# Kernel tuning notes

Hardware: AMD Instinct MI355X
Metric: run time of the kernel (lower is better)

Reference implementation:

```python
import jax, jax.numpy as jnp
import numpy as np

B, S, D, H = 2, 2048, 1024, 16
HD = D // H

def setup_inputs() -> dict:
    key = jax.random.key(0)
    ks = jax.random.split(key, 5)
    scale = 0.02
    return {
        "x": jax.random.normal(ks[0], (B, S, D), dtype=jnp.float32),
        "Wq": jax.random.normal(ks[1], (D, D), dtype=jnp.float32) * scale,
        "Wk": jax.random.normal(ks[2], (D, D), dtype=jnp.float32) * scale,
        "Wv": jax.random.normal(ks[3], (D, D), dtype=jnp.float32) * scale,
        "Wo": jax.random.normal(ks[4], (D, D), dtype=jnp.float32) * scale,
        "bo": jnp.zeros((D,), dtype=jnp.float32),
    }

def reference(x, Wq, Wk, Wv, Wo, bo):
    b, n, _ = x.shape
    h, hd = H, HD
    # QKV projections (torch Linear: x @ W.T)
    q = (x @ Wq.T).reshape(b, n, h, hd).transpose(0, 2, 1, 3)  # [b,h,n,hd]
    k = (x @ Wk.T).reshape(b, n, h, hd).transpose(0, 2, 1, 3)
    v = (x @ Wv.T).reshape(b, n, h, hd).transpose(0, 2, 1, 3)
    scores = jnp.einsum("bhqd,bhkd->bhqk", q, k) / jnp.sqrt(jnp.float32(hd))
    # causal mask: positions j > i masked out
    causal = jnp.tril(jnp.ones((n, n), dtype=bool))
    scores = jnp.where(causal, scores, jnp.float32(-jnp.inf))
    attn = jax.nn.softmax(scores, axis=-1)  # dropout p=0.0 (eval)
    ctx = jnp.einsum("bhqk,bhkd->bhqd", attn, v)
    ctx = ctx.transpose(0, 2, 1, 3).reshape(b, n, h * hd)
    return ctx @ Wo.T + bo
```

## Files before the change

kernel.cpp:

```cpp
#include <hip/hip_runtime.h>
#include <stdint.h>

typedef __attribute__((ext_vector_type(8))) short short8;
typedef __attribute__((ext_vector_type(4))) short s16x4;
typedef __attribute__((ext_vector_type(4))) float f32x4;
typedef __attribute__((ext_vector_type(4))) uint32_t u32x4;

#define B_ 2
#define S_ 2048
#define D_ 1024
#define H_ 16
#define HD_ 64
#define BS_ (B_ * S_)
#define QKVN (3 * D_)
#define QKN 2048
#define XN8 (BS_ * D_ / 8)
#define WN8 (D_ * D_ / 8)

#define NEGBIG (-1e30f)

__device__ __forceinline__ short f2bf(float f) {
    uint32_t u = __builtin_bit_cast(uint32_t, f);
    u = (u + 0x7FFFu + ((u >> 16) & 1u)) >> 16;
    return (short)u;
}

__device__ __forceinline__ uint32_t cvtpk_bf16(float lo, float hi) {
    uint32_t r;
    asm("v_cvt_pk_bf16_f32 %0, %1, %2" : "=v"(r) : "v"(lo), "v"(hi));
    return r;
}

__device__ __forceinline__ void gload_lds16(const void* g, void* lds) {
    __builtin_amdgcn_global_load_lds(
        (const __attribute__((address_space(1))) void*)g,
        (__attribute__((address_space(3))) void*)lds, 16, 0, 0);
}

__global__ void castall(const float* __restrict__ x, const float* __restrict__ Wq,
                        const float* __restrict__ Wk, const float* __restrict__ Wv,
                        const float* __restrict__ Wo, short* __restrict__ dst,
                        float qs) {
    int i = blockIdx.x * blockDim.x + threadIdx.x;
    int stride = gridDim.x * blockDim.x;
    const int total = XN8 + 4 * WN8;
    for (; i < total; i += stride) {
        const float* s;
        int loc;
        float sc = 1.f;
        if (i < XN8) {
            s = x; loc = i;
        } else {
            int r = i - XN8;
            int wi = r >> 17;
            loc = r & (WN8 - 1);
            s = (wi == 0) ? Wq : (wi == 1) ? Wk : (wi == 2) ? Wv : Wo;
            if (wi == 0) sc = qs;
        }
        const float* sp = s + (size_t)loc * 8;
        short8 o;
#pragma unroll
        for (int j = 0; j < 8; ++j) o[j] = f2bf(sp[j] * sc);
        *(short8*)(dst + (size_t)i * 8) = o;
    }
}

template <int MODE>
__global__ __launch_bounds__(256) void gemm_nt(
    const short* __restrict__ A, const short* __restrict__ Bt,
    void* __restrict__ Cout, const float* __restrict__ bias,
    short* __restrict__ vtg, int M, int N, int K) {
    __shared__ short As[128 * 64];
    __shared__ short Bs[128 * 64];
    const int tid = threadIdx.x;
    const int w = tid >> 6, l = tid & 63;
    const int lg = l >> 4, lr = l & 15;
    const int nbn = N >> 7;
    const int bm = blockIdx.x / nbn, bn = blockIdx.x % nbn;
    const int m0 = bm << 7, n0 = bn << 7;
    const int wm = (w >> 1) << 6, wn = (w & 1) << 6;

    f32x4 acc[4][4] = {};

    for (int kt = 0; kt < K; kt += 64) {
#pragma unroll
        for (int it = 0; it < 4; ++it) {
            int off = ((it * 4 + w) * 64 + l) * 16;
            int row = off >> 7;
            int scol = (off & 127) ^ ((row & 7) << 4);
            gload_lds16(A + (size_t)(m0 + row) * K + kt + (scol >> 1),
                        (char*)As + (it * 4 + w) * 1024);
            gload_lds16(Bt + (size_t)(n0 + row) * K + kt + (scol >> 1),
                        (char*)Bs + (it * 4 + w) * 1024);
        }
        __syncthreads();
        short8 af[4][2], bf[4][2];
#pragma unroll
        for (int f = 0; f < 4; ++f)
#pragma unroll
            for (int ks = 0; ks < 2; ++ks) {
                int ra = wm + f * 16 + lr;
                af[f][ks] = *(const short8*)((const char*)As + ra * 128 +
                                             ((lg * 16 + ks * 64) ^ ((ra & 7) << 4)));
                int rb = wn + f * 16 + lr;
                bf[f][ks] = *(const short8*)((const char*)Bs + rb * 128 +
                                             ((lg * 16 + ks * 64) ^ ((rb & 7) << 4)));
            }
#pragma unroll
        for (int mf = 0; mf < 4; ++mf)
#pragma unroll
            for (int nf = 0; nf < 4; ++nf)
#pragma unroll
                for (int ks = 0; ks < 2; ++ks)
                    acc[mf][nf] = __builtin_amdgcn_mfma_f32_16x16x32_bf16(
                        af[mf][ks], bf[nf][ks], acc[mf][nf], 0, 0, 0);
        __syncthreads();
    }

    if (MODE == 2 && n0 >= QKN) {
#pragma unroll
        for (int mf = 0; mf < 4; ++mf)
#pragma unroll
            for (int nf = 0; nf < 4; ++nf) {
                int col = n0 + wn + nf * 16 + lr - QKN;
                int hh = col >> 6, d = col & 63;
                int token = m0 + wm + mf * 16 + lg * 4;
                int b = token >> 11, tk = token & 2047;
                int t64 = tk & ~63, rem = tk & 63;
                int r32 = rem & 31;
                int pos = (rem >> 5) * 32 + ((r32 & 15) >> 2) * 8 + ((r32 >> 4) & 1) * 4;
                s16x4 o;
#pragma unroll
                for (int i = 0; i < 4; ++i) o[i] = f2bf(acc[mf][nf][i]);
                *(s16x4*)&vtg[((size_t)(b * 16 + hh) * 64 + d) * (size_t)S_ + t64 + pos] = o;
            }
        return;
    }

#pragma unroll
    for (int mf = 0; mf < 4; ++mf)
#pragma unroll
        for (int nf = 0; nf < 4; ++nf) {
            int col = n0 + wn + nf * 16 + lr;
            float bv = 0.f;
            if (MODE == 1) bv = bias[col];
#pragma unroll
            for (int i = 0; i < 4; ++i) {
                int row = m0 + wm + mf * 16 + lg * 4 + i;
                float v = acc[mf][nf][i] + bv;
                if (MODE == 1)
                    ((float*)Cout)[(size_t)row * N + col] = v;
                else
                    ((short*)Cout)[(size_t)row * QKN + col] = f2bf(v);
            }
        }
}

__global__ __launch_bounds__(256) void attn_fwd(const short* __restrict__ qkb,
                                                const short* __restrict__ vtg,
                                                short* __restrict__ ctx) {
    const int qt = (S_ / 64 - 1) - blockIdx.x;
    const int bh = blockIdx.y;
    const int b = bh >> 4, h = bh & 15;
    const int tid = threadIdx.x;
    const int w = tid >> 6, l = tid & 63;
    const int lg = l >> 4, lr = l & 15;
    const int q0w = qt * 64 + w * 16;

    __shared__ short Ks[2][64 * 64];
    __shared__ short Vt[2][64 * 64];

    const short* base = qkb + (size_t)(b * S_) * QKN + h * HD_;
    const short* kpg = base + D_;
    const short* vrow = vtg + (size_t)bh * 64 * S_;

    short8 qf[2];
    {
        const short* g = base + (size_t)(q0w + lr) * QKN + lg * 8;
        qf[0] = *(const short8*)g;
        qf[1] = *(const short8*)(g + 32);
    }

    int off0 = (w * 64 + l) * 16, off1 = ((4 + w) * 64 + l) * 16;
    int row0 = off0 >> 7, row1 = off1 >> 7;
    int sc0 = (off0 & 127) ^ ((row0 & 7) << 4);
    int sc1 = (off1 & 127) ^ ((row1 & 7) << 4);
    const short* kA = kpg + (size_t)row0 * QKN + (sc0 >> 1);
    const short* kB = kpg + (size_t)row1 * QKN + (sc1 >> 1);
    const short* vA = vrow + (size_t)row0 * S_ + (sc0 >> 1);
    const short* vB = vrow + (size_t)row1 * S_ + (sc1 >> 1);
    char* ldsKA[2] = {(char*)Ks[0] + w * 1024, (char*)Ks[1] + w * 1024};
    char* ldsKB[2] = {(char*)Ks[0] + (4 + w) * 1024, (char*)Ks[1] + (4 + w) * 1024};
    char* ldsVA[2] = {(char*)Vt[0] + w * 1024, (char*)Vt[1] + w * 1024};
    char* ldsVB[2] = {(char*)Vt[0] + (4 + w) * 1024, (char*)Vt[1] + (4 + w) * 1024};

    auto stage = [&](int buf) {
        gload_lds16(kA, ldsKA[buf]);
        gload_lds16(kB, ldsKB[buf]);
        gload_lds16(vA, ldsVA[buf]);
        gload_lds16(vB, ldsVB[buf]);
        kA += 64 * QKN; kB += 64 * QKN; vA += 64; vB += 64;
    };

    float m2 = NEGBIG, lsum = 0.f;
    f32x4 cacc[4] = {};
    const int qabs = q0w + lr;

    stage(0);
    __syncthreads();

    for (int kt = 0; kt <= qt; ++kt) {
        const int buf = kt & 1;
        if (kt < qt) stage(buf ^ 1);

        const char* ksb = (const char*)Ks[buf];
        const char* vtb = (const char*)Vt[buf];

        f32x4 sfr[4] = {};
#pragma unroll
        for (int f = 0; f < 4; ++f)
#pragma unroll
            for (int ks = 0; ks < 2; ++ks) {
                int r = f * 16 + lr;
                short8 kf = *(const short8*)(ksb + r * 128 +
                                             ((lg * 16 + ks * 64) ^ ((r & 7) << 4)));
                sfr[f] = __builtin_amdgcn_mfma_f32_16x16x32_bf16(kf, qf[ks], sfr[f], 0, 0, 0);
            }

        float p[16];
        if (kt == qt) {
            const int kb = kt * 64;
#pragma unroll
            for (int f = 0; f < 4; ++f)
#pragma unroll
                for (int i = 0; i < 4; ++i) {
                    int kpo = kb + f * 16 + lg * 4 + i;
                    p[f * 4 + i] = (kpo <= qabs) ? sfr[f][i] : NEGBIG;
                }
        } else {
#pragma unroll
            for (int f = 0; f < 4; ++f)
#pragma unroll
                for (int i = 0; i < 4; ++i) p[f * 4 + i] = sfr[f][i];
        }
        float mx01 = fmaxf(fmaxf(p[0], p[1]), fmaxf(p[2], p[3]));
        float mx23 = fmaxf(fmaxf(p[4], p[5]), fmaxf(p[6], p[7]));
        float mx45 = fmaxf(fmaxf(p[8], p[9]), fmaxf(p[10], p[11]));
        float mx67 = fmaxf(fmaxf(p[12], p[13]), fmaxf(p[14], p[15]));
        float tmax = fmaxf(fmaxf(mx01, mx23), fmaxf(mx45, mx67));

        if (!__all(tmax - m2 <= 8.f)) {
            float rmax = fmaxf(tmax, __shfl_xor(tmax, 16));
            rmax = fmaxf(rmax, __shfl_xor(rmax, 32));
            float mnew = fmaxf(m2, rmax);
            float crs = exp2f(m2 - mnew);
            m2 = mnew;
            lsum *= crs;
#pragma unroll
            for (int i = 0; i < 4; ++i) {
                float ci = __shfl(crs, lg * 4 + i);
#pragma unroll
                for (int nf = 0; nf < 4; ++nf) cacc[nf][i] *= ci;
            }
        }
#pragma unroll
        for (int t = 0; t < 16; ++t) p[t] = exp2f(p[t] - m2);
        float s0 = (p[0] + p[1]) + (p[2] + p[3]);
        float s1 = (p[4] + p[5]) + (p[6] + p[7]);
        float s2 = (p[8] + p[9]) + (p[10] + p[11]);
        float s3 = (p[12] + p[13]) + (p[14] + p[15]);
        lsum += (s0 + s1) + (s2 + s3);

        short8 pa[2];
#pragma unroll
        for (int ks = 0; ks < 2; ++ks) {
            u32x4 pw;
#pragma unroll
            for (int wd = 0; wd < 4; ++wd) {
                int tb = (2 * ks + (wd >> 1)) * 4 + (wd & 1) * 2;
                pw[wd] = cvtpk_bf16(p[tb], p[tb + 1]);
            }
            pa[ks] = __builtin_bit_cast(short8, pw);
        }

#pragma unroll
        for (int nf = 0; nf < 4; ++nf) {
            int r = nf * 16 + lr;
#pragma unroll
            for (int ks = 0; ks < 2; ++ks) {
                short8 vf = *(const short8*)(vtb + r * 128 +
                                             ((ks * 64 + lg * 16) ^ ((r & 7) << 4)));
                cacc[nf] = __builtin_amdgcn_mfma_f32_16x16x32_bf16(pa[ks], vf, cacc[nf], 0, 0, 0);
            }
        }
        __syncthreads();
    }

    lsum += __shfl_xor(lsum, 16);
    lsum += __shfl_xor(lsum, 32);
    float inv = 1.0f / lsum;
#pragma unroll
    for (int i = 0; i < 4; ++i) {
        float li = __shfl(inv, lg * 4 + i);
        int srow = q0w + lg * 4 + i;
        short* o = ctx + (size_t)(b * S_ + srow) * D_ + h * HD_ + lr;
#pragma unroll
        for (int nf = 0; nf < 4; ++nf) o[nf * 16] = f2bf(cacc[nf][i] * li);
    }
}

extern "C" void kernel_launch(void* const* d_in, const int* in_sizes, int n_in,
                              void* d_out, int out_size, void* d_ws, size_t ws_size,
                              hipStream_t stream) {
    const float* x  = (const float*)d_in[0];
    const float* Wq = (const float*)d_in[1];
    const float* Wk = (const float*)d_in[2];
    const float* Wv = (const float*)d_in[3];
    const float* Wo = (const float*)d_in[4];
    const float* bo = (const float*)d_in[5];

    short* xb   = (short*)d_ws;
    short* Wqkv = xb + (size_t)BS_ * D_;
    short* Wob  = Wqkv + (size_t)QKVN * D_;
    short* qkb  = Wob + (size_t)D_ * D_;
    short* ctxb = qkb + (size_t)BS_ * QKN;
    short* vtg  = ctxb + (size_t)BS_ * D_;

    const float qscale = 0.125f * 1.44269504089f;
    castall<<<2048, 256, 0, stream>>>(x, Wq, Wk, Wv, Wo, (short*)d_ws, qscale);

    gemm_nt<2><<<dim3((BS_ / 128) * (QKVN / 128)), 256, 0, stream>>>(
        xb, Wqkv, qkb, nullptr, vtg, BS_, QKVN, D_);

    attn_fwd<<<dim3(S_ / 64, B_ * H_), 256, 0, stream>>>(qkb, vtg, ctxb);

    gemm_nt<1><<<dim3((BS_ / 128) * (D_ / 128)), 256, 0, stream>>>(
        ctxb, Wob, d_out, bo, nullptr, BS_, D_, D_);
}
```

Measured before the change: 217.2 us.

## Pair high and low causal query tiles per attention block to share K/V loads

Each attention block now handles two query tiles, one near the end of the sequence and its mirror near the start, giving every block the same amount of causal work. Each staged K/V tile is reused for both query tiles while the low tile is still active, which halves the K/V traffic for that stretch and halves the grid size. The K and V fragments are preloaded into registers, and exp2f is replaced with the raw v_exp_f32 instruction. The cost is higher register pressure from two sets of accumulators, and a grid of only 512 blocks may leave some compute units underused.

New measurement: 187.7 us. -13.6%, faster.

```diff
diff --git a/kernel.cpp b/kernel.cpp
--- a/kernel.cpp
+++ b/kernel.cpp
@@ -28,6 +28,12 @@
 __device__ __forceinline__ uint32_t cvtpk_bf16(float lo, float hi) {
     uint32_t r;
     asm("v_cvt_pk_bf16_f32 %0, %1, %2" : "=v"(r) : "v"(lo), "v"(hi));
+    return r;
+}
+
+__device__ __forceinline__ float vexp2(float x) {
+    float r;
+    asm("v_exp_f32 %0, %1" : "=v"(r) : "v"(x));
     return r;
 }
 
@@ -159,26 +165,29 @@
 __global__ __launch_bounds__(256) void attn_fwd(const short* __restrict__ qkb,
                                                 const short* __restrict__ vtg,
                                                 short* __restrict__ ctx) {
-    const int qt = (S_ / 64 - 1) - blockIdx.x;
+    const int bx = blockIdx.x;
+    const int qtH = (S_ / 64 - 1) - bx;
+    const int qtL = bx;
     const int bh = blockIdx.y;
     const int b = bh >> 4, h = bh & 15;
     const int tid = threadIdx.x;
     const int w = tid >> 6, l = tid & 63;
     const int lg = l >> 4, lr = l & 15;
-    const int q0w = qt * 64 + w * 16;
-
-    __shared__ short Ks[2][64 * 64];
-    __shared__ short Vt[2][64 * 64];
+
+    __shared__ __align__(16) char lds[32768];
 
     const short* base = qkb + (size_t)(b * S_) * QKN + h * HD_;
     const short* kpg = base + D_;
     const short* vrow = vtg + (size_t)bh * 64 * S_;
 
-    short8 qf[2];
+    short8 qfH[2], qfL[2];
     {
-        const short* g = base + (size_t)(q0w + lr) * QKN + lg * 8;
-        qf[0] = *(const short8*)g;
-        qf[1] = *(const short8*)(g + 32);
+        const short* g = base + (size_t)(qtH * 64 + w * 16 + lr) * QKN + lg * 8;
+        qfH[0] = *(const short8*)g;
+        qfH[1] = *(const short8*)(g + 32);
+        const short* g2 = base + (size_t)(qtL * 64 + w * 16 + lr) * QKN + lg * 8;
+        qfL[0] = *(const short8*)g2;
+        qfL[1] = *(const short8*)(g2 + 32);
     }
 
     int off0 = (w * 64 + l) * 16, off1 = ((4 + w) * 64 + l) * 16;
@@ -189,124 +198,145 @@
     const short* kB = kpg + (size_t)row1 * QKN + (sc1 >> 1);
     const short* vA = vrow + (size_t)row0 * S_ + (sc0 >> 1);
     const short* vB = vrow + (size_t)row1 * S_ + (sc1 >> 1);
-    char* ldsKA[2] = {(char*)Ks[0] + w * 1024, (char*)Ks[1] + w * 1024};
-    char* ldsKB[2] = {(char*)Ks[0] + (4 + w) * 1024, (char*)Ks[1] + (4 + w) * 1024};
-    char* ldsVA[2] = {(char*)Vt[0] + w * 1024, (char*)Vt[1] + w * 1024};
-    char* ldsVB[2] = {(char*)Vt[0] + (4 + w) * 1024, (char*)Vt[1] + (4 + w) * 1024};
+    const int dK0 = w * 1024, dK1 = (4 + w) * 1024;
 
     auto stage = [&](int buf) {
-        gload_lds16(kA, ldsKA[buf]);
-        gload_lds16(kB, ldsKB[buf]);
-        gload_lds16(vA, ldsVA[buf]);
-        gload_lds16(vB, ldsVB[buf]);
+        char* p = lds + (buf << 14);
+        gload_lds16(kA, p + dK0);
+        gload_lds16(kB, p + dK1);
+        gload_lds16(vA, p + 8192 + dK0);
+        gload_lds16(vB, p + 8192 + dK1);
         kA += 64 * QKN; kB += 64 * QKN; vA += 64; vB += 64;
     };
 
-    float m2 = NEGBIG, lsum = 0.f;
-    f32x4 cacc[4] = {};
-    const int qabs = q0w + lr;
+    const int xorp = (lr & 7) << 4;
+    const int ka0 = lr * 128 + ((lg * 16) ^ xorp);
+    const int ka1 = lr * 128 + ((lg * 16 + 64) ^ xorp);
+    const int va0 = 8192 + ka0;
+    const int va1 = 8192 + ka1;
+
+    float mH = NEGBIG, lsH = 0.f, mL = NEGBIG, lsL = 0.f;
+    f32x4 caccH[4] = {}, caccL[4] = {};
+    const int qrow = w * 16 + lr;
+    const int qabsH = qtH * 64 + qrow;
+    const int qabsL = qtL * 64 + qrow;
 
     stage(0);
     __syncthreads();
 
-    for (int kt = 0; kt <= qt; ++kt) {
+    for (int kt = 0; kt <= qtH; ++kt) {
         const int buf = kt & 1;
-        if (kt < qt) stage(buf ^ 1);
-
-        const char* ksb = (const char*)Ks[buf];
-        const char* vtb = (const char*)Vt[buf];
-
-        f32x4 sfr[4] = {};
-#pragma unroll
-        for (int f = 0; f < 4; ++f)
+        if (kt < qtH) stage(buf ^ 1);
+        const char* bb = lds + (buf << 14);
+        const bool doL = (kt <= qtL);
+
+        short8 kf[4][2];
+#pragma unroll
+        for (int f = 0; f < 4; ++f) {
+            kf[f][0] = *(const short8*)(bb + ka0 + f * 2048);
+            kf[f][1] = *(const short8*)(bb + ka1 + f * 2048);
+        }
+        f32x4 sH[4] = {};
+#pragma unroll
+        for (int f = 0; f < 4; ++f) {
+            sH[f] = __builtin_amdgcn_mfma_f32_16x16x32_bf16(kf[f][0], qfH[0], sH[f], 0, 0, 0);
+            sH[f] = __builtin_amdgcn_mfma_f32_16x16x32_bf16(kf[f][1], qfH[1], sH[f], 0, 0, 0);
+        }
+        f32x4 sL[4] = {};
+        if (doL) {
+#pragma unroll
+            for (int f = 0; f < 4; ++f) {
+                sL[f] = __builtin_amdgcn_mfma_f32_16x16x32_bf16(kf[f][0], qfL[0], sL[f], 0, 0, 0);
+                sL[f] = __builtin_amdgcn_mfma_f32_16x16x32_bf16(kf[f][1], qfL[1], sL[f], 0, 0, 0);
+            }
+        }
+        short8 vf[4][2];
+#pragma unroll
+        for (int nf = 0; nf < 4; ++nf) {
+            vf[nf][0] = *(const short8*)(bb + va0 + nf * 2048);
+            vf[nf][1] = *(const short8*)(bb + va1 + nf * 2048);
+        }
+
+        auto smpv = [&](f32x4(&sfr)[4], float& m2, float& lsum, f32x4(&cacc)[4],
+                        int qabs, bool diag) {
+            float p[16];
+            if (diag) {
+                int rel = qabs - kt * 64;
+#pragma unroll
+                for (int f = 0; f < 4; ++f)
+#pragma unroll
+                    for (int i = 0; i < 4; ++i)
+                        p[f * 4 + i] = (f * 16 + lg * 4 + i <= rel) ? sfr[f][i] : NEGBIG;
+            } else {
+#pragma unroll
+                for (int f = 0; f < 4; ++f)
+#pragma unroll
+                    for (int i = 0; i < 4; ++i) p[f * 4 + i] = sfr[f][i];
+            }
+            float t0 = fmaxf(fmaxf(p[0], p[1]), fmaxf(p[2], p[3]));
+            float t1 = fmaxf(fmaxf(p[4], p[5]), fmaxf(p[6], p[7]));
+            float t2 = fmaxf(fmaxf(p[8], p[9]), fmaxf(p[10], p[11]));
+            float t3 = fmaxf(fmaxf(p[12], p[13]), fmaxf(p[14], p[15]));
+            float tmax = fmaxf(fmaxf(t0, t1), fmaxf(t2, t3));
+            if (!__all(tmax - m2 <= 8.f)) {
+                float rmax = fmaxf(tmax, __shfl_xor(tmax, 16));
+                rmax = fmaxf(rmax, __shfl_xor(rmax, 32));
+                float mnew = fmaxf(m2, rmax);
+                float crs = vexp2(m2 - mnew);
+                m2 = mnew;
+                lsum *= crs;
+#pragma unroll
+                for (int i = 0; i < 4; ++i) {
+                    float ci = __shfl(crs, lg * 4 + i);
+#pragma unroll
+                    for (int nf = 0; nf < 4; ++nf) cacc[nf][i] *= ci;
+                }
+            }
+#pragma unroll
+            for (int t = 0; t < 16; ++t) p[t] = vexp2(p[t] - m2);
+            float s0 = (p[0] + p[1]) + (p[2] + p[3]);
+            float s1 = (p[4] + p[5]) + (p[6] + p[7]);
+            float s2 = (p[8] + p[9]) + (p[10] + p[11]);
+            float s3 = (p[12] + p[13]) + (p[14] + p[15]);
+            lsum += (s0 + s1) + (s2 + s3);
+            short8 pa[2];
 #pragma unroll
             for (int ks = 0; ks < 2; ++ks) {
-                int r = f * 16 + lr;
-                short8 kf = *(const short8*)(ksb + r * 128 +
-                                             ((lg * 16 + ks * 64) ^ ((r & 7) << 4)));
-                sfr[f] = __builtin_amdgcn_mfma_f32_16x16x32_bf16(kf, qf[ks], sfr[f], 0, 0, 0);
-            }
-
-        float p[16];
-        if (kt == qt) {
-            const int kb = kt * 64;
-#pragma unroll
-            for (int f = 0; f < 4; ++f)
-#pragma unroll
-                for (int i = 0; i < 4; ++i) {
-                    int kpo = kb + f * 16 + lg * 4 + i;
-                    p[f * 4 + i] = (kpo <= qabs) ? sfr[f][i] : NEGBIG;
+                u32x4 pw;
+#pragma unroll
+                for (int wd = 0; wd < 4; ++wd) {
+                    int tb = (2 * ks + (wd >> 1)) * 4 + (wd & 1) * 2;
+                    pw[wd] = cvtpk_bf16(p[tb], p[tb + 1]);
                 }
-        } else {
-#pragma unroll
-            for (int f = 0; f < 4; ++f)
-#pragma unroll
-                for (int i = 0; i < 4; ++i) p[f * 4 + i] = sfr[f][i];
-        }
-        float mx01 = fmaxf(fmaxf(p[0], p[1]), fmaxf(p[2], p[3]));
-        float mx23 = fmaxf(fmaxf(p[4], p[5]), fmaxf(p[6], p[7]));
-        float mx45 = fmaxf(fmaxf(p[8], p[9]), fmaxf(p[10], p[11]));
-        float mx67 = fmaxf(fmaxf(p[12], p[13]), fmaxf(p[14], p[15]));
-        float tmax = fmaxf(fmaxf(mx01, mx23), fmaxf(mx45, mx67));
-
-        if (!__all(tmax - m2 <= 8.f)) {
-            float rmax = fmaxf(tmax, __shfl_xor(tmax, 16));
-            rmax = fmaxf(rmax, __shfl_xor(rmax, 32));
-            float mnew = fmaxf(m2, rmax);
-            float crs = exp2f(m2 - mnew);
-            m2 = mnew;
-            lsum *= crs;
-#pragma unroll
-            for (int i = 0; i < 4; ++i) {
-                float ci = __shfl(crs, lg * 4 + i);
-#pragma unroll
-                for (int nf = 0; nf < 4; ++nf) cacc[nf][i] *= ci;
-            }
-        }
-#pragma unroll
-        for (int t = 0; t < 16; ++t) p[t] = exp2f(p[t] - m2);
-        float s0 = (p[0] + p[1]) + (p[2] + p[3]);
-        float s1 = (p[4] + p[5]) + (p[6] + p[7]);
-        float s2 = (p[8] + p[9]) + (p[10] + p[11]);
-        float s3 = (p[12] + p[13]) + (p[14] + p[15]);
-        lsum += (s0 + s1) + (s2 + s3);
-
-        short8 pa[2];
-#pragma unroll
-        for (int ks = 0; ks < 2; ++ks) {
-            u32x4 pw;
-#pragma unroll
-            for (int wd = 0; wd < 4; ++wd) {
-                int tb = (2 * ks + (wd >> 1)) * 4 + (wd & 1) * 2;
-                pw[wd] = cvtpk_bf16(p[tb], p[tb + 1]);
-            }
-            pa[ks] = __builtin_bit_cast(short8, pw);
-        }
-
-#pragma unroll
-        for (int nf = 0; nf < 4; ++nf) {
-            int r = nf * 16 + lr;
-#pragma unroll
-            for (int ks = 0; ks < 2; ++ks) {
-                short8 vf = *(const short8*)(vtb + r * 128 +
-                                             ((ks * 64 + lg * 16) ^ ((r & 7) << 4)));
-                cacc[nf] = __builtin_amdgcn_mfma_f32_16x16x32_bf16(pa[ks], vf, cacc[nf], 0, 0, 0);
-            }
-        }
+                pa[ks] = __builtin_bit_cast(short8, pw);
+            }
+#pragma unroll
+            for (int nf = 0; nf < 4; ++nf) {
+                cacc[nf] = __builtin_amdgcn_mfma_f32_16x16x32_bf16(pa[0], vf[nf][0], cacc[nf], 0, 0, 0);
+                cacc[nf] = __builtin_amdgcn_mfma_f32_16x16x32_bf16(pa[1], vf[nf][1], cacc[nf], 0, 0, 0);
+            }
+        };
+
+        smpv(sH, mH, lsH, caccH, qabsH, kt == qtH);
+        if (doL) smpv(sL, mL, lsL, caccL, qabsL, kt == qtL);
         __syncthreads();
     }
 
-    lsum += __shfl_xor(lsum, 16);
-    lsum += __shfl_xor(lsum, 32);
-    float inv = 1.0f / lsum;
-#pragma unroll
-    for (int i = 0; i < 4; ++i) {
-        float li = __shfl(inv, lg * 4 + i);
-        int srow = q0w + lg * 4 + i;
-        short* o = ctx + (size_t)(b * S_ + srow) * D_ + h * HD_ + lr;
-#pragma unroll
-        for (int nf = 0; nf < 4; ++nf) o[nf * 16] = f2bf(cacc[nf][i] * li);
-    }
+    auto finish = [&](float lsum, f32x4(&cacc)[4], int qt) {
+        float ls = lsum + __shfl_xor(lsum, 16);
+        ls += __shfl_xor(ls, 32);
+        float inv = 1.0f / ls;
+#pragma unroll
+        for (int i = 0; i < 4; ++i) {
+            float li = __shfl(inv, lg * 4 + i);
+            int srow = qt * 64 + w * 16 + lg * 4 + i;
+            short* o = ctx + (size_t)(b * S_ + srow) * D_ + h * HD_ + lr;
+#pragma unroll
+            for (int nf = 0; nf < 4; ++nf) o[nf * 16] = f2bf(cacc[nf][i] * li);
+        }
+    };
+    finish(lsH, caccH, qtH);
+    finish(lsL, caccL, qtL);
 }
 
 extern "C" void kernel_launch(void* const* d_in, const int* in_sizes, int n_in,
@@ -332,7 +362,7 @@
     gemm_nt<2><<<dim3((BS_ / 128) * (QKVN / 128)), 256, 0, stream>>>(
         xb, Wqkv, qkb, nullptr, vtg, BS_, QKVN, D_);
 
-    attn_fwd<<<dim3(S_ / 64, B_ * H_), 256, 0, stream>>>(qkb, vtg, ctxb);
+    attn_fwd<<<dim3(S_ / 128, B_ * H_), 256, 0, stream>>>(qkb, vtg, ctxb);
 
     gemm_nt<1><<<dim3((BS_ / 128) * (D_ / 128)), 256, 0, stream>>>(
         ctxb, Wob, d_out, bo, nullptr, BS_, D_, D_);
```
